# Kernel tuning notes

Hardware: AMD Instinct MI355X
Metric: run time of the kernel (lower is better)

Reference implementation:

```python
import jax, jax.numpy as jnp
import numpy as np
import math

# config constants (match init_kwargs)
H = 1024; NH = 16; NKV = 4; HD = 64; E = 16; I = 512
NG = 4; TKG = 2; TK = 4; ROUTED_SCALE = 2.5; EPS = 1e-6; THETA = 10000.0
B = 2; S = 1024


def setup_inputs() -> dict:
    key = jax.random.key(0)
    ks = jax.random.split(key, 16)
    sd = 0.02
    inp = {
        "hidden_states": jax.random.normal(ks[0], (B, S, H), jnp.float32),
        "position_ids": jnp.arange(B * S, dtype=jnp.int64).reshape(B, S) % 4096,
        "ln1_w": jnp.ones((H,), jnp.float32),
        "ln2_w": jnp.ones((H,), jnp.float32),
        "q_w": jax.random.normal(ks[1], (NH * HD, H), jnp.float32) * sd,
        "k_w": jax.random.normal(ks[2], (NKV * HD, H), jnp.float32) * sd,
        "v_w": jax.random.normal(ks[3], (NKV * HD, H), jnp.float32) * sd,
        "o_w": jax.random.normal(ks[4], (H, NH * HD), jnp.float32) * sd,
        "gate_w": jax.random.normal(ks[5], (E, H), jnp.float32) * sd,
        "e_bias": jax.random.normal(ks[6], (E,), jnp.float32) * 0.1,
        "W_gu": jax.random.normal(ks[7], (E, 2 * I, H), jnp.float32) * sd,
        "W_d": jax.random.normal(ks[8], (E, H, I), jnp.float32) * sd,
        "sg_w": jax.random.normal(ks[9], (2 * I, H), jnp.float32) * sd,
        "su_w": jax.random.normal(ks[10], (2 * I, H), jnp.float32) * sd,
        "sd_w": jax.random.normal(ks[11], (H, 2 * I), jnp.float32) * sd,
    }
    return inp


def _rmsnorm(x, w, eps=EPS):
    v = jnp.mean(x.astype(jnp.float32) ** 2, axis=-1, keepdims=True)
    return w * (x * jax.lax.rsqrt(v + eps)).astype(w.dtype)


def _rotate_half(x):
    x1, x2 = x[..., : HD // 2], x[..., HD // 2 :]
    return jnp.concatenate([-x2, x1], axis=-1)


def _attention(hs, position_ids, q_w, k_w, v_w, o_w):
    b, s, _ = hs.shape
    q = (hs @ q_w.T).reshape(b, s, NH, HD).transpose(0, 2, 1, 3)   # [B,NH,S,HD]
    k = (hs @ k_w.T).reshape(b, s, NKV, HD).transpose(0, 2, 1, 3)
    v = (hs @ v_w.T).reshape(b, s, NKV, HD).transpose(0, 2, 1, 3)
    # RoPE
    inv_freq = 1.0 / (THETA ** (jnp.arange(0, HD, 2, dtype=jnp.float32) / HD))
    freqs = position_ids.astype(jnp.float32)[..., None] * inv_freq  # [B,S,HD/2]
    emb = jnp.concatenate([freqs, freqs], axis=-1)                  # [B,S,HD]
    cos = jnp.cos(emb)[:, None]                                     # [B,1,S,HD]
    sin = jnp.sin(emb)[:, None]
    q = q * cos + _rotate_half(q) * sin
    k = k * cos + _rotate_half(k) * sin
    # GQA: repeat kv heads
    groups = NH // NKV
    k = jnp.repeat(k, groups, axis=1)
    v = jnp.repeat(v, groups, axis=1)
    scale = 1.0 / math.sqrt(HD)
    scores = jnp.einsum("bhsd,bhtd->bhst", q, k) * scale
    causal = jnp.triu(jnp.full((s, s), -jnp.inf, jnp.float32), k=1)
    scores = scores + causal[None, None]
    attn = jax.nn.softmax(scores.astype(jnp.float32), axis=-1).astype(q.dtype)
    out = jnp.einsum("bhst,bhtd->bhsd", attn, v)
    out = out.transpose(0, 2, 1, 3).reshape(b, s, NH * HD)
    return out @ o_w.T


def _moe(x, gate_w, e_bias, W_gu, W_d, sg_w, su_w, sd_w):
    b, s, h = x.shape
    xf = x.reshape(-1, h)                                     # [T,H]
    T = xf.shape[0]
    logits = xf.astype(jnp.float32) @ gate_w.astype(jnp.float32).T  # [T,E]
    scores = jax.nn.sigmoid(logits)
    sfc = scores + e_bias[None]
    # group-restricted top-k
    gsize = E // NG
    group_scores = sfc.reshape(T, NG, gsize).max(axis=-1)     # [T,NG]
    _, gidx = jax.lax.top_k(group_scores, TKG)                # [T,TKG]
    gmask = jnp.zeros((T, NG), bool).at[jnp.arange(T)[:, None], gidx].set(True)
    smask = jnp.repeat(gmask, gsize, axis=1)                  # [T,E]
    masked = jnp.where(smask, sfc, 0.0)
    _, topk_idx = jax.lax.top_k(masked, TK)                   # [T,TK]
    topk_w = jnp.take_along_axis(scores, topk_idx, axis=1)    # [T,TK]
    topk_w = topk_w / (topk_w.sum(axis=-1, keepdims=True) + 1e-20)
    topk_w = (topk_w * ROUTED_SCALE).astype(xf.dtype)
    # combine weights [T,E] (scatter-add over selected experts)
    combine = jnp.zeros((T, E), xf.dtype).at[
        jnp.arange(T)[:, None], topk_idx].add(topk_w)
    # dense expert compute (static shapes), weighted combine fused in einsum
    gu = jnp.einsum("th,eih->tei", xf, W_gu)                  # [T,E,2I]
    hidden = jax.nn.silu(gu[..., :I]) * gu[..., I:]           # [T,E,I]
    routed = jnp.einsum("tei,ehi,te->th", hidden, W_d, combine)
    # shared experts
    shared = ((jax.nn.silu(xf @ sg_w.T) * (xf @ su_w.T)) @ sd_w.T)
    return (routed + shared).reshape(b, s, h)


def reference(hidden_states, position_ids, ln1_w, ln2_w, q_w, k_w, v_w, o_w,
              gate_w, e_bias, W_gu, W_d, sg_w, su_w, sd_w):
    res = hidden_states
    hs = _rmsnorm(hidden_states, ln1_w)
    hs = res + _attention(hs, position_ids, q_w, k_w, v_w, o_w)
    res = hs
    hs = _rmsnorm(hs, ln2_w)
    hs = res + _moe(hs, gate_w, e_bias, W_gu, W_d, sg_w, su_w, sd_w)
    return hs
```

## Files before the change

### kernel.cpp

```cpp
#include <hip/hip_runtime.h>
#include <hip/hip_bf16.h>
#include <stdint.h>

typedef float f32x4 __attribute__((ext_vector_type(4)));
typedef short s16x8 __attribute__((ext_vector_type(8)));
typedef short s16x4 __attribute__((ext_vector_type(4)));

__device__ __forceinline__ short f2bf(float x) {
    union { float f; uint32_t u; } v; v.f = x;
    uint32_t r = v.u + 0x7fffu + ((v.u >> 16) & 1u);
    return (short)(r >> 16);
}
__device__ __forceinline__ float bf2f(short b) {
    union { uint32_t u; float f; } v; v.u = ((uint32_t)(uint16_t)b) << 16;
    return v.f;
}
__device__ __forceinline__ void gld16(const void* g, void* l) {
    __builtin_amdgcn_global_load_lds((const __attribute__((address_space(1))) uint32_t*)g,
                                     (__attribute__((address_space(3))) uint32_t*)l, 16, 0, 0);
}

__global__ __launch_bounds__(256) void cvt_all_kernel(const float* __restrict__ q, const float* __restrict__ k,
                                                      const float* __restrict__ v, const float* __restrict__ o,
                                                      const float* __restrict__ gu, const float* __restrict__ wd,
                                                      const float* __restrict__ sg, const float* __restrict__ su,
                                                      const float* __restrict__ sd, short* __restrict__ wqkv,
                                                      short* __restrict__ wo, short* __restrict__ wgu,
                                                      short* __restrict__ wdB, short* __restrict__ wsgsu,
                                                      short* __restrict__ wsd) {
    size_t i = (size_t)blockIdx.x * 256 + threadIdx.x;
    const float* src; short* dst;
    if (i < 655360) {
        if (i < 262144) { src = q + i * 4; dst = wqkv + i * 4; }
        else if (i < 327680) { src = k + (i - 262144) * 4; dst = wqkv + 1048576 + (i - 262144) * 4; }
        else if (i < 393216) { src = v + (i - 327680) * 4; dst = wqkv + 1310720 + (i - 327680) * 4; }
        else { src = o + (i - 393216) * 4; dst = wo + (i - 393216) * 4; }
    } else if (i < 6946816) {
        if (i < 4849664) { src = gu + (i - 655360) * 4; dst = wgu + (i - 655360) * 4; }
        else { src = wd + (i - 4849664) * 4; dst = wdB + (i - 4849664) * 4; }
    } else {
        if (i < 7208960) { src = sg + (i - 6946816) * 4; dst = wsgsu + (i - 6946816) * 4; }
        else if (i < 7471104) { src = su + (i - 7208960) * 4; dst = wsgsu + 1048576 + (i - 7208960) * 4; }
        else { src = sd + (i - 7471104) * 4; dst = wsd + (i - 7471104) * 4; }
    }
    f32x4 val = *(const f32x4*)src;
    s16x4 ov;
    ov[0] = f2bf(val[0]); ov[1] = f2bf(val[1]); ov[2] = f2bf(val[2]); ov[3] = f2bf(val[3]);
    *(s16x4*)dst = ov;
}

__global__ __launch_bounds__(256) void rmsnorm_kernel(const float* __restrict__ x, const float* __restrict__ w,
                                                      short* __restrict__ out) {
    int t = blockIdx.x;
    f32x4 v = ((const f32x4*)(x + (size_t)t * 1024))[threadIdx.x];
    float ssq = v[0]*v[0] + v[1]*v[1] + v[2]*v[2] + v[3]*v[3];
#pragma unroll
    for (int o = 1; o < 64; o <<= 1) ssq += __shfl_xor(ssq, o);
    __shared__ float red[4];
    if ((threadIdx.x & 63) == 0) red[threadIdx.x >> 6] = ssq;
    __syncthreads();
    float tot = red[0] + red[1] + red[2] + red[3];
    float rs = rsqrtf(tot * (1.0f / 1024.0f) + 1e-6f);
    f32x4 wv = ((const f32x4*)w)[threadIdx.x];
    s16x4 o4;
#pragma unroll
    for (int j = 0; j < 4; ++j) o4[j] = f2bf(v[j] * rs * wv[j]);
    ((s16x4*)(out + (size_t)t * 1024))[threadIdx.x] = o4;
}

__global__ __launch_bounds__(256) void addnorm_kernel(const float* __restrict__ a, const float* __restrict__ b,
                                                      const float* __restrict__ w, float* __restrict__ res,
                                                      short* __restrict__ xf, float* __restrict__ xf32) {
    int t = blockIdx.x;
    f32x4 va = ((const f32x4*)(a + (size_t)t * 1024))[threadIdx.x];
    f32x4 vb = ((const f32x4*)(b + (size_t)t * 1024))[threadIdx.x]
             + ((const f32x4*)(b + (size_t)2048 * 1024 + (size_t)t * 1024))[threadIdx.x];
    f32x4 s = va + vb;
    ((f32x4*)(res + (size_t)t * 1024))[threadIdx.x] = s;
    float ssq = s[0]*s[0] + s[1]*s[1] + s[2]*s[2] + s[3]*s[3];
#pragma unroll
    for (int o = 1; o < 64; o <<= 1) ssq += __shfl_xor(ssq, o);
    __shared__ float red[4];
    if ((threadIdx.x & 63) == 0) red[threadIdx.x >> 6] = ssq;
    __syncthreads();
    float tot = red[0] + red[1] + red[2] + red[3];
    float rs = rsqrtf(tot * (1.0f / 1024.0f) + 1e-6f);
    f32x4 wv = ((const f32x4*)w)[threadIdx.x];
    f32x4 xo;
    s16x4 o4;
#pragma unroll
    for (int j = 0; j < 4; ++j) { xo[j] = s[j] * rs * wv[j]; o4[j] = f2bf(xo[j]); }
    ((f32x4*)(xf32 + (size_t)t * 1024))[threadIdx.x] = xo;
    ((s16x4*)(xf + (size_t)t * 1024))[threadIdx.x] = o4;
}

__global__ __launch_bounds__(256, 4) void gemm2_kernel(const short* __restrict__ A, const short* __restrict__ Bg,
                                                       void* __restrict__ Cv, int M, int N, int Ktot, int Ksub,
                                                       const int* __restrict__ counts, const int* __restrict__ lists,
                                                       const int* __restrict__ plan, int a_shift, int store_bf16) {
    __shared__ short As[2][128 * 32];
    __shared__ short Bs[2][128 * 32];
    int e, bm, bn, k0, Mloc;
    size_t coff;
    const int* rl = nullptr;
    if (plan) {
        int wi = blockIdx.y;
        if (wi >= plan[0]) return;
        int it = plan[1 + wi];
        e = it & 31; bm = (it >> 5) * 128;
        bn = blockIdx.x * 128; k0 = 0;
        Mloc = counts[e]; rl = lists + e * 2048; coff = 0;
    } else {
        e = 0; bm = blockIdx.x * 128; bn = blockIdx.y * 128;
        k0 = blockIdx.z * Ksub; Mloc = M;
        coff = (size_t)blockIdx.z * M * N;
    }
    if (bm >= Mloc) return;
    const short* Bt = Bg + (size_t)e * N * Ktot;
    int tid = threadIdx.x, w = tid >> 6, l = tid & 63;
    int lr = l & 15, lg = l >> 4;
    int rsub = l >> 2, u = l & 3;
    int fs = (rsub & 3) ^ ((rsub >> 2) & 3);
    int colsel = (u ^ fs) * 8;
    int ra = w * 32 + rsub;
    int ga0 = bm + ra;       if (ga0 > Mloc - 1) ga0 = Mloc - 1;
    int ga1 = bm + ra + 16;  if (ga1 > Mloc - 1) ga1 = Mloc - 1;
    int ar0 = rl ? (rl[ga0] >> a_shift) : ga0;
    int ar1 = rl ? (rl[ga1] >> a_shift) : ga1;
    const short* Ap0 = A + (size_t)ar0 * Ktot + k0 + colsel;
    const short* Ap1 = A + (size_t)ar1 * Ktot + k0 + colsel;
    const short* Bp0 = Bt + (size_t)(bn + ra) * Ktot + k0 + colsel;
    const short* Bp1 = Bt + (size_t)(bn + ra + 16) * Ktot + k0 + colsel;
    int lb0 = w * 1024, lb1 = w * 1024 + 512;

    int wm = (w >> 1) * 64, wn = (w & 1) * 64;
    int su = lg ^ (lr & 3) ^ ((lr >> 2) & 3);
    int aoff[4], boff[4];
#pragma unroll
    for (int mf = 0; mf < 4; ++mf) aoff[mf] = (wm + mf * 16 + lr) * 32 + su * 8;
#pragma unroll
    for (int nf = 0; nf < 4; ++nf) boff[nf] = (wn + nf * 16 + lr) * 32 + su * 8;

    f32x4 zero4 = {0.f, 0.f, 0.f, 0.f};
    f32x4 acc[4][4];
#pragma unroll
    for (int mf = 0; mf < 4; ++mf)
#pragma unroll
        for (int nf = 0; nf < 4; ++nf) acc[mf][nf] = zero4;

#define STAGE(buf, kt) do { \
        gld16(Ap0 + (kt) * 32, &As[buf][lb0]); \
        gld16(Ap1 + (kt) * 32, &As[buf][lb1]); \
        gld16(Bp0 + (kt) * 32, &Bs[buf][lb0]); \
        gld16(Bp1 + (kt) * 32, &Bs[buf][lb1]); \
    } while (0)

    int nk = Ksub >> 5;
    STAGE(0, 0);
    asm volatile("s_waitcnt vmcnt(0)");
    __syncthreads();
    for (int kt = 0; kt < nk; ++kt) {
        int cur = kt & 1;
        if (kt + 1 < nk) STAGE(cur ^ 1, kt + 1);
        s16x8 af[4], bfr[4];
#pragma unroll
        for (int mf = 0; mf < 4; ++mf) af[mf] = *(const s16x8*)&As[cur][aoff[mf]];
#pragma unroll
        for (int nf = 0; nf < 4; ++nf) bfr[nf] = *(const s16x8*)&Bs[cur][boff[nf]];
#pragma unroll
        for (int mf = 0; mf < 4; ++mf)
#pragma unroll
            for (int nf = 0; nf < 4; ++nf)
                acc[mf][nf] = __builtin_amdgcn_mfma_f32_16x16x32_bf16(af[mf], bfr[nf], acc[mf][nf], 0, 0, 0);
        __syncthreads();
    }
#undef STAGE
    float* Cf = (float*)Cv;
    short* Cs = (short*)Cv;
#pragma unroll
    for (int mf = 0; mf < 4; ++mf) {
        int rbase = bm + wm + mf * 16 + lg * 4;
#pragma unroll
        for (int r = 0; r < 4; ++r) {
            int grow = rbase + r;
            if (grow < Mloc) {
                int crow = rl ? rl[grow] : grow;
                size_t cb = coff + (size_t)crow * N + bn + wn + lr;
                if (store_bf16) {
#pragma unroll
                    for (int nf = 0; nf < 4; ++nf) Cs[cb + nf * 16] = f2bf(acc[mf][nf][r]);
                } else {
#pragma unroll
                    for (int nf = 0; nf < 4; ++nf) Cf[cb + nf * 16] = acc[mf][nf][r];
                }
            }
        }
    }
}

__global__ __launch_bounds__(64) void rope_kernel(const float* __restrict__ qkv, short* __restrict__ Qr,
                                                  short* __restrict__ Kr, short* __restrict__ Vt) {
    int t = blockIdx.x;
    int b = t >> 10, s = t & 1023;
    int l = threadIdx.x;
    __shared__ float cs[32], sn[32], qrow[1024], krow[256], vrow[256];
    const f32x4* r0 = (const f32x4*)(qkv + (size_t)t * 1536);
    const f32x4* r1 = (const f32x4*)(qkv + (size_t)2048 * 1536 + (size_t)t * 1536);
#pragma unroll
    for (int i = 0; i < 4; ++i) ((f32x4*)qrow)[l + i * 64] = r0[l + i * 64] + r1[l + i * 64];
    ((f32x4*)krow)[l] = r0[256 + l] + r1[256 + l];
    ((f32x4*)vrow)[l] = r0[320 + l] + r1[320 + l];
    if (l < 32) {
        float fr = (float)t * exp2f(-(float)l * 0.41524101186f);
        cs[l] = cosf(fr); sn[l] = sinf(fr);
    }
    __syncthreads();
    int d = l;
    float c = cs[d & 31], sv = sn[d & 31];
#pragma unroll
    for (int h = 0; h < 16; ++h) {
        float x = qrow[h * 64 + d];
        float rot = (d < 32) ? -qrow[h * 64 + d + 32] : qrow[h * 64 + d - 32];
        Qr[((size_t)(b * 16 + h) * 1024 + s) * 64 + d] = f2bf((x * c + rot * sv) * 0.125f);
    }
#pragma unroll
    for (int h = 0; h < 4; ++h) {
        float x = krow[h * 64 + d];
        float rot = (d < 32) ? -krow[h * 64 + d + 32] : krow[h * 64 + d - 32];
        Kr[((size_t)(b * 4 + h) * 1024 + s) * 64 + d] = f2bf(x * c + rot * sv);
        Vt[((size_t)(b * 4 + h) * 64 + d) * 1024 + s] = f2bf(vrow[h * 64 + d]);
    }
}

__global__ __launch_bounds__(64) void attn_kernel(const short* __restrict__ Qr, const short* __restrict__ Kr,
                                                  const short* __restrict__ Vt, short* __restrict__ attn_out) {
    int qb = blockIdx.x;
    int hb = blockIdx.y;
    int b = hb >> 4, h = hb & 15, kv = h >> 2;
    int l = threadIdx.x;
    int lr = l & 15, lg = l >> 4;
    int q0 = qb * 16;
    __shared__ short Pl[16 * 32];
    const short* Qbase = Qr + ((size_t)(b * 16 + h) * 1024 + q0 + lr) * 64;
    s16x8 qf0 = *(const s16x8*)(Qbase + lg * 8);
    s16x8 qf1 = *(const s16x8*)(Qbase + 32 + lg * 8);
    const short* Kbase = Kr + (size_t)(b * 4 + kv) * 1024 * 64;
    const short* Vbase = Vt + (size_t)(b * 4 + kv) * 64 * 1024;

    f32x4 zero4 = {0.f, 0.f, 0.f, 0.f};
    f32x4 o[4];
#pragma unroll
    for (int dt = 0; dt < 4; ++dt) o[dt] = zero4;
    float m = -1e30f, lsum = 0.f;
    int nt = (q0 + 16 + 31) >> 5;
    for (int kt = 0; kt < nt; ++kt) {
        int k0 = kt * 32;
        f32x4 sc0 = zero4, sc1 = zero4;
        const short* Kr0 = Kbase + (size_t)(k0 + lr) * 64;
        s16x8 ka = *(const s16x8*)(Kr0 + lg * 8);
        sc0 = __builtin_amdgcn_mfma_f32_16x16x32_bf16(ka, qf0, sc0, 0, 0, 0);
        ka = *(const s16x8*)(Kr0 + 32 + lg * 8);
        sc0 = __builtin_amdgcn_mfma_f32_16x16x32_bf16(ka, qf1, sc0, 0, 0, 0);
        const short* Kr1 = Kbase + (size_t)(k0 + 16 + lr) * 64;
        ka = *(const s16x8*)(Kr1 + lg * 8);
        sc1 = __builtin_amdgcn_mfma_f32_16x16x32_bf16(ka, qf0, sc1, 0, 0, 0);
        ka = *(const s16x8*)(Kr1 + 32 + lg * 8);
        sc1 = __builtin_amdgcn_mfma_f32_16x16x32_bf16(ka, qf1, sc1, 0, 0, 0);
        if (kt == nt - 1) {
            int q = q0 + lr;
#pragma unroll
            for (int r = 0; r < 4; ++r) {
                if (k0 + lg * 4 + r > q) sc0[r] = -1e30f;
                if (k0 + 16 + lg * 4 + r > q) sc1[r] = -1e30f;
            }
        }
        float tm = fmaxf(fmaxf(fmaxf(sc0[0], sc0[1]), fmaxf(sc0[2], sc0[3])),
                         fmaxf(fmaxf(sc1[0], sc1[1]), fmaxf(sc1[2], sc1[3])));
        tm = fmaxf(tm, __shfl_xor(tm, 16));
        tm = fmaxf(tm, __shfl_xor(tm, 32));
        float newm = fmaxf(m, tm);
        float fac = __expf(m - newm);
        float p[8];
#pragma unroll
        for (int r = 0; r < 4; ++r) { p[r] = __expf(sc0[r] - newm); p[4 + r] = __expf(sc1[r] - newm); }
        float ts = ((p[0] + p[1]) + (p[2] + p[3])) + ((p[4] + p[5]) + (p[6] + p[7]));
        ts += __shfl_xor(ts, 16);
        ts += __shfl_xor(ts, 32);
        lsum = lsum * fac + ts;
        m = newm;
        s16x4 w0, w1;
#pragma unroll
        for (int r = 0; r < 4; ++r) { w0[r] = f2bf(p[r]); w1[r] = f2bf(p[4 + r]); }
        *(s16x4*)&Pl[lr * 32 + lg * 4] = w0;
        *(s16x4*)&Pl[lr * 32 + 16 + lg * 4] = w1;
#pragma unroll
        for (int dt = 0; dt < 4; ++dt) {
            const short* Vrow = Vbase + (size_t)(dt * 16 + lr) * 1024 + k0;
            s16x8 va = *(const s16x8*)(Vrow + lg * 8);
            s16x8 pf = *(const s16x8*)&Pl[lr * 32 + lg * 8];
            o[dt] *= fac;
            o[dt] = __builtin_amdgcn_mfma_f32_16x16x32_bf16(va, pf, o[dt], 0, 0, 0);
        }
    }
    float inv = 1.f / lsum;
    short* obase = attn_out + ((size_t)(b * 1024 + q0 + lr)) * 1024 + h * 64;
#pragma unroll
    for (int dt = 0; dt < 4; ++dt)
#pragma unroll
        for (int r = 0; r < 4; ++r) obase[dt * 16 + lg * 4 + r] = f2bf(o[dt][r] * inv);
}

__global__ __launch_bounds__(256) void router_topk_kernel(const float* __restrict__ x32, const float* __restrict__ gw,
                                                          const float* __restrict__ eb, float* __restrict__ tw,
                                                          int* __restrict__ tidx) {
    int t = blockIdx.x * 4 + (threadIdx.x >> 6);
    int l = threadIdx.x & 63;
    const float* x = x32 + (size_t)t * 1024;
    f32x4 xv[4];
#pragma unroll
    for (int j = 0; j < 4; ++j) xv[j] = *(const f32x4*)(x + j * 256 + l * 4);
    float acc[16];
#pragma unroll
    for (int e = 0; e < 16; ++e) {
        float a = 0.f;
#pragma unroll
        for (int j = 0; j < 4; ++j) {
            f32x4 g = *(const f32x4*)(gw + (size_t)e * 1024 + j * 256 + l * 4);
            a += xv[j][0]*g[0] + xv[j][1]*g[1] + xv[j][2]*g[2] + xv[j][3]*g[3];
        }
        acc[e] = a;
    }
#pragma unroll
    for (int e = 0; e < 16; ++e) {
#pragma unroll
        for (int o = 1; o < 64; o <<= 1) acc[e] += __shfl_xor(acc[e], o);
    }
    if (l == 0) {
        float score[16], sfc[16];
#pragma unroll
        for (int e = 0; e < 16; ++e) {
            score[e] = 1.f / (1.f + __expf(-acc[e]));
            sfc[e] = score[e] + eb[e];
        }
        float gs[4];
#pragma unroll
        for (int g = 0; g < 4; ++g)
            gs[g] = fmaxf(fmaxf(sfc[4 * g], sfc[4 * g + 1]), fmaxf(sfc[4 * g + 2], sfc[4 * g + 3]));
        int g1 = 0;
        for (int g = 1; g < 4; ++g) if (gs[g] > gs[g1]) g1 = g;
        int g2 = -1;
        for (int g = 0; g < 4; ++g) {
            if (g == g1) continue;
            if (g2 < 0 || gs[g] > gs[g2]) g2 = g;
        }
        float masked[16];
#pragma unroll
        for (int e = 0; e < 16; ++e) {
            int g = e >> 2;
            masked[e] = (g == g1 || g == g2) ? sfc[e] : 0.0f;
        }
        float tot = 1e-20f;
        int idx[4]; float wv[4];
        for (int k = 0; k < 4; ++k) {
            int bi = 0;
            float bv = -1e30f;
            for (int e2 = 0; e2 < 16; ++e2)
                if (masked[e2] > bv) { bv = masked[e2]; bi = e2; }
            idx[k] = bi;
            wv[k] = score[bi];
            masked[bi] = -1e30f;
            tot += wv[k];
        }
        for (int k = 0; k < 4; ++k) {
            tw[t * 4 + k] = wv[k] / tot * 2.5f;
            tidx[t * 4 + k] = idx[k];
        }
    }
}

__global__ __launch_bounds__(64) void router_lists_kernel(const int* __restrict__ tidx, int* __restrict__ counts,
                                                          int* __restrict__ lists) {
    int e = blockIdx.x;
    int l = threadIdx.x;
    int base = 0;
    for (int it = 0; it < 128; ++it) {
        int p = it * 64 + l;
        bool match = (tidx[p] == e);
        unsigned long long mask = __ballot(match);
        int pos = __popcll(mask & ((1ull << l) - 1ull));
        if (match) lists[e * 2048 + base + pos] = p;
        base += __popcll(mask);
    }
    if (l == 0) counts[e] = base;
}

__global__ void plan_kernel(const int* __restrict__ counts, int* __restrict__ plan) {
    if (threadIdx.x == 0) {
        int n = 0;
        for (int e = 0; e < 16; ++e) {
            int nb = (counts[e] + 127) >> 7;
            for (int m2 = 0; m2 < nb; ++m2) plan[1 + n++] = e | (m2 << 5);
        }
        plan[0] = n;
    }
}

__global__ __launch_bounds__(128) void silu_routed_kernel(const short* __restrict__ gu, short* __restrict__ hid) {
    int pr = blockIdx.x;
    int j = threadIdx.x * 4;
    s16x4 gv = *(const s16x4*)(gu + (size_t)pr * 1024 + j);
    s16x4 uv = *(const s16x4*)(gu + (size_t)pr * 1024 + 512 + j);
    s16x4 o;
#pragma unroll
    for (int k = 0; k < 4; ++k) {
        float gf = bf2f(gv[k]);
        o[k] = f2bf(gf / (1.f + __expf(-gf)) * bf2f(uv[k]));
    }
    *(s16x4*)(hid + (size_t)pr * 512 + j) = o;
}

__global__ __launch_bounds__(256) void silu_shared_kernel(const short* __restrict__ gu, short* __restrict__ h) {
    int t = blockIdx.x;
    int j = threadIdx.x * 4;
    s16x4 gv = *(const s16x4*)(gu + (size_t)t * 2048 + j);
    s16x4 uv = *(const s16x4*)(gu + (size_t)t * 2048 + 1024 + j);
    s16x4 o;
#pragma unroll
    for (int k = 0; k < 4; ++k) {
        float gf = bf2f(gv[k]);
        o[k] = f2bf(gf / (1.f + __expf(-gf)) * bf2f(uv[k]));
    }
    *(s16x4*)(h + (size_t)t * 1024 + j) = o;
}

__global__ __launch_bounds__(256) void combine_kernel(const float* __restrict__ res2, const float* __restrict__ sdp,
                                                      const short* __restrict__ slots, const float* __restrict__ tw,
                                                      float* __restrict__ out) {
    int t = blockIdx.x;
    int i = threadIdx.x;
    f32x4 a = ((const f32x4*)(res2 + (size_t)t * 1024))[i];
    f32x4 s0 = ((const f32x4*)(sdp + (size_t)t * 1024))[i];
    f32x4 s1 = ((const f32x4*)(sdp + (size_t)2048 * 1024 + (size_t)t * 1024))[i];
    f32x4 acc = a + s0 + s1;
#pragma unroll
    for (int s = 0; s < 4; ++s) {
        float w = tw[t * 4 + s];
        s16x4 d = ((const s16x4*)(slots + (size_t)(t * 4 + s) * 1024))[i];
#pragma unroll
        for (int j = 0; j < 4; ++j) acc[j] += bf2f(d[j]) * w;
    }
    ((f32x4*)(out + (size_t)t * 1024))[i] = acc;
}

extern "C" void kernel_launch(void* const* d_in, const int* in_sizes, int n_in,
                              void* d_out, int out_size, void* d_ws, size_t ws_size,
                              hipStream_t stream) {
    const float* hidden = (const float*)d_in[0];
    const float* ln1 = (const float*)d_in[2];
    const float* ln2 = (const float*)d_in[3];
    const float* qw = (const float*)d_in[4];
    const float* kw = (const float*)d_in[5];
    const float* vw = (const float*)d_in[6];
    const float* ow = (const float*)d_in[7];
    const float* gatew = (const float*)d_in[8];
    const float* ebias = (const float*)d_in[9];
    const float* wgu = (const float*)d_in[10];
    const float* wd = (const float*)d_in[11];
    const float* sgw = (const float*)d_in[12];
    const float* suw = (const float*)d_in[13];
    const float* sdw = (const float*)d_in[14];
    float* out = (float*)d_out;

    char* base = (char*)d_ws;
    size_t off = 0;
    auto alloc = [&](size_t bytes) -> char* {
        char* r = base + off;
        off += (bytes + 255) & ~(size_t)255;
        return r;
    };
    const size_t MB = 1u << 20;

    short* wqkv_b = (short*)alloc((size_t)1536 * 1024 * 2);
    short* wo_b   = (short*)alloc((size_t)1024 * 1024 * 2);
    short* wgu_b  = (short*)alloc((size_t)16 * 1024 * 1024 * 2);
    short* wd_b   = (short*)alloc((size_t)16 * 1024 * 512 * 2);
    short* wsgsu_b= (short*)alloc((size_t)2048 * 1024 * 2);
    short* wsd_b  = (short*)alloc((size_t)1024 * 1024 * 2);
    float* res2 = (float*)alloc((size_t)2048 * 1024 * 4);
    short* xf   = (short*)alloc((size_t)2048 * 1024 * 2);
    float* topkw = (float*)alloc(2048 * 4 * 4);
    int* tidx   = (int*)alloc(8192 * 4);
    int* counts = (int*)alloc(64);
    int* lists  = (int*)alloc(16 * 2048 * 4);
    int* plan   = (int*)alloc(512);
    short* gu_or_sgsu = (short*)alloc((size_t)8192 * 1024 * 2);
    short* shhid = (short*)alloc((size_t)2048 * 1024 * 2);
    short* hid   = (short*)alloc((size_t)8192 * 512 * 2);

    char* ov = alloc(50 * MB);
    short* xn1       = (short*)(ov);
    float* qkv_part  = (float*)(ov + 4 * MB);
    short* Qr        = (short*)(ov);
    short* Kr        = (short*)(ov + 28 * MB);
    short* Vt        = (short*)(ov + 29 * MB);
    short* attn_out  = (short*)(ov + 30 * MB);
    float* attnproj_part = (float*)(ov + 34 * MB);
    float* xf32      = (float*)(ov);
    short* down_slot = (short*)(ov + 8 * MB);
    float* sd_part   = (float*)(ov + 24 * MB);

    cvt_all_kernel<<<30208, 256, 0, stream>>>(qw, kw, vw, ow, wgu, wd, sgw, suw, sdw,
                                              wqkv_b, wo_b, wgu_b, wd_b, wsgsu_b, wsd_b);

    rmsnorm_kernel<<<2048, 256, 0, stream>>>(hidden, ln1, xn1);
    gemm2_kernel<<<dim3(16, 12, 2), 256, 0, stream>>>(xn1, wqkv_b, qkv_part, 2048, 1536, 1024, 512,
                                                      nullptr, nullptr, nullptr, 0, 0);
    rope_kernel<<<2048, 64, 0, stream>>>(qkv_part, Qr, Kr, Vt);
    attn_kernel<<<dim3(64, 32, 1), 64, 0, stream>>>(Qr, Kr, Vt, attn_out);
    gemm2_kernel<<<dim3(16, 8, 2), 256, 0, stream>>>(attn_out, wo_b, attnproj_part, 2048, 1024, 1024, 512,
                                                     nullptr, nullptr, nullptr, 0, 0);
    addnorm_kernel<<<2048, 256, 0, stream>>>(hidden, attnproj_part, ln2, res2, xf, xf32);

    router_topk_kernel<<<512, 256, 0, stream>>>(xf32, gatew, ebias, topkw, tidx);
    router_lists_kernel<<<16, 64, 0, stream>>>(tidx, counts, lists);
    plan_kernel<<<1, 64, 0, stream>>>(counts, plan);

    gemm2_kernel<<<dim3(16, 16, 1), 256, 0, stream>>>(xf, wsgsu_b, gu_or_sgsu, 2048, 2048, 1024, 1024,
                                                      nullptr, nullptr, nullptr, 0, 1);
    silu_shared_kernel<<<2048, 256, 0, stream>>>(gu_or_sgsu, shhid);

    gemm2_kernel<<<dim3(8, 80, 1), 256, 0, stream>>>(xf, wgu_b, gu_or_sgsu, 0, 1024, 1024, 1024,
                                                     counts, lists, plan, 2, 1);
    silu_routed_kernel<<<8192, 128, 0, stream>>>(gu_or_sgsu, hid);

    gemm2_kernel<<<dim3(8, 80, 1), 256, 0, stream>>>(hid, wd_b, down_slot, 0, 1024, 512, 512,
                                                     counts, lists, plan, 0, 1);
    gemm2_kernel<<<dim3(16, 8, 2), 256, 0, stream>>>(shhid, wsd_b, sd_part, 2048, 1024, 1024, 512,
                                                     nullptr, nullptr, nullptr, 0, 0);

    combine_kernel<<<2048, 256, 0, stream>>>(res2, sd_part, down_slot, topkw, out);

    (void)in_sizes; (void)n_in; (void)out_size; (void)ws_size;
}
```

Baseline: 325.4 us.

## Pair mirrored causal query tiles per attention block with double-buffered K/V loads

Each attention block now handles two 16-row query tiles, p and 63-p, so causal work is balanced across blocks and every K/V tile loaded is reused by both query tiles. K/V fragments for the next key tile are prefetched into registers (double buffer) while the current tile is computed, and the P scratch in LDS is padded to 40 shorts per row. The grid is halved, so there are fewer and longer blocks, and register pressure rises from the two accumulator sets plus the buffered K/V fragments.

```diff
diff --git a/kernel.cpp b/kernel.cpp
--- a/kernel.cpp
+++ b/kernel.cpp
@@ -232,82 +232,110 @@
     }
 }
 
+struct KV { s16x8 k[4]; s16x8 v[4]; };
+__device__ __forceinline__ void kv_load(KV& r, const short* Kb, const short* Vb, int k0, int lr, int lg) {
+    const short* K0 = Kb + (size_t)(k0 + lr) * 64 + lg * 8;
+    const short* K1 = Kb + (size_t)(k0 + 16 + lr) * 64 + lg * 8;
+    r.k[0] = *(const s16x8*)K0;
+    r.k[1] = *(const s16x8*)(K0 + 32);
+    r.k[2] = *(const s16x8*)K1;
+    r.k[3] = *(const s16x8*)(K1 + 32);
+#pragma unroll
+    for (int dt = 0; dt < 4; ++dt)
+        r.v[dt] = *(const s16x8*)(Vb + (size_t)(dt * 16 + lr) * 1024 + k0 + lg * 8);
+}
+__device__ __forceinline__ void chain_step(const KV& kv, s16x8 qf0, s16x8 qf1, f32x4* o,
+                                           float& m, float& lsum, short* Pl,
+                                           int lr, int lg, int k0, int qmask) {
+    f32x4 z = {0.f, 0.f, 0.f, 0.f};
+    f32x4 sc0 = z, sc1 = z;
+    sc0 = __builtin_amdgcn_mfma_f32_16x16x32_bf16(kv.k[0], qf0, sc0, 0, 0, 0);
+    sc0 = __builtin_amdgcn_mfma_f32_16x16x32_bf16(kv.k[1], qf1, sc0, 0, 0, 0);
+    sc1 = __builtin_amdgcn_mfma_f32_16x16x32_bf16(kv.k[2], qf0, sc1, 0, 0, 0);
+    sc1 = __builtin_amdgcn_mfma_f32_16x16x32_bf16(kv.k[3], qf1, sc1, 0, 0, 0);
+#pragma unroll
+    for (int r = 0; r < 4; ++r) {
+        if (k0 + lg * 4 + r > qmask) sc0[r] = -1e30f;
+        if (k0 + 16 + lg * 4 + r > qmask) sc1[r] = -1e30f;
+    }
+    float tm = fmaxf(fmaxf(fmaxf(sc0[0], sc0[1]), fmaxf(sc0[2], sc0[3])),
+                     fmaxf(fmaxf(sc1[0], sc1[1]), fmaxf(sc1[2], sc1[3])));
+    tm = fmaxf(tm, __shfl_xor(tm, 16));
+    tm = fmaxf(tm, __shfl_xor(tm, 32));
+    float newm = fmaxf(m, tm);
+    float fac = __expf(m - newm);
+    float p[8];
+#pragma unroll
+    for (int r = 0; r < 4; ++r) { p[r] = __expf(sc0[r] - newm); p[4 + r] = __expf(sc1[r] - newm); }
+    float ts = ((p[0] + p[1]) + (p[2] + p[3])) + ((p[4] + p[5]) + (p[6] + p[7]));
+    ts += __shfl_xor(ts, 16);
+    ts += __shfl_xor(ts, 32);
+    lsum = lsum * fac + ts;
+    m = newm;
+    s16x4 w0, w1;
+#pragma unroll
+    for (int r = 0; r < 4; ++r) { w0[r] = f2bf(p[r]); w1[r] = f2bf(p[4 + r]); }
+    *(s16x4*)&Pl[lr * 40 + lg * 4] = w0;
+    *(s16x4*)&Pl[lr * 40 + 16 + lg * 4] = w1;
+    s16x8 pf = *(const s16x8*)&Pl[lr * 40 + lg * 8];
+#pragma unroll
+    for (int dt = 0; dt < 4; ++dt) {
+        o[dt] *= fac;
+        o[dt] = __builtin_amdgcn_mfma_f32_16x16x32_bf16(kv.v[dt], pf, o[dt], 0, 0, 0);
+    }
+}
+
 __global__ __launch_bounds__(64) void attn_kernel(const short* __restrict__ Qr, const short* __restrict__ Kr,
                                                   const short* __restrict__ Vt, short* __restrict__ attn_out) {
-    int qb = blockIdx.x;
+    int p = blockIdx.x;
     int hb = blockIdx.y;
     int b = hb >> 4, h = hb & 15, kv = h >> 2;
     int l = threadIdx.x;
     int lr = l & 15, lg = l >> 4;
-    int q0 = qb * 16;
-    __shared__ short Pl[16 * 32];
-    const short* Qbase = Qr + ((size_t)(b * 16 + h) * 1024 + q0 + lr) * 64;
-    s16x8 qf0 = *(const s16x8*)(Qbase + lg * 8);
-    s16x8 qf1 = *(const s16x8*)(Qbase + 32 + lg * 8);
+    int q0A = p * 16, q0B = (63 - p) * 16;
+    __shared__ short PlA[16 * 40], PlB[16 * 40];
+    const short* Qh = Qr + (size_t)(b * 16 + h) * 1024 * 64;
+    s16x8 qA0 = *(const s16x8*)(Qh + (size_t)(q0A + lr) * 64 + lg * 8);
+    s16x8 qA1 = *(const s16x8*)(Qh + (size_t)(q0A + lr) * 64 + 32 + lg * 8);
+    s16x8 qB0 = *(const s16x8*)(Qh + (size_t)(q0B + lr) * 64 + lg * 8);
+    s16x8 qB1 = *(const s16x8*)(Qh + (size_t)(q0B + lr) * 64 + 32 + lg * 8);
     const short* Kbase = Kr + (size_t)(b * 4 + kv) * 1024 * 64;
     const short* Vbase = Vt + (size_t)(b * 4 + kv) * 64 * 1024;
 
     f32x4 zero4 = {0.f, 0.f, 0.f, 0.f};
-    f32x4 o[4];
-#pragma unroll
-    for (int dt = 0; dt < 4; ++dt) o[dt] = zero4;
-    float m = -1e30f, lsum = 0.f;
-    int nt = (q0 + 16 + 31) >> 5;
-    for (int kt = 0; kt < nt; ++kt) {
-        int k0 = kt * 32;
-        f32x4 sc0 = zero4, sc1 = zero4;
-        const short* Kr0 = Kbase + (size_t)(k0 + lr) * 64;
-        s16x8 ka = *(const s16x8*)(Kr0 + lg * 8);
-        sc0 = __builtin_amdgcn_mfma_f32_16x16x32_bf16(ka, qf0, sc0, 0, 0, 0);
-        ka = *(const s16x8*)(Kr0 + 32 + lg * 8);
-        sc0 = __builtin_amdgcn_mfma_f32_16x16x32_bf16(ka, qf1, sc0, 0, 0, 0);
-        const short* Kr1 = Kbase + (size_t)(k0 + 16 + lr) * 64;
-        ka = *(const s16x8*)(Kr1 + lg * 8);
-        sc1 = __builtin_amdgcn_mfma_f32_16x16x32_bf16(ka, qf0, sc1, 0, 0, 0);
-        ka = *(const s16x8*)(Kr1 + 32 + lg * 8);
-        sc1 = __builtin_amdgcn_mfma_f32_16x16x32_bf16(ka, qf1, sc1, 0, 0, 0);
-        if (kt == nt - 1) {
-            int q = q0 + lr;
-#pragma unroll
-            for (int r = 0; r < 4; ++r) {
-                if (k0 + lg * 4 + r > q) sc0[r] = -1e30f;
-                if (k0 + 16 + lg * 4 + r > q) sc1[r] = -1e30f;
-            }
-        }
-        float tm = fmaxf(fmaxf(fmaxf(sc0[0], sc0[1]), fmaxf(sc0[2], sc0[3])),
-                         fmaxf(fmaxf(sc1[0], sc1[1]), fmaxf(sc1[2], sc1[3])));
-        tm = fmaxf(tm, __shfl_xor(tm, 16));
-        tm = fmaxf(tm, __shfl_xor(tm, 32));
-        float newm = fmaxf(m, tm);
-        float fac = __expf(m - newm);
-        float p[8];
-#pragma unroll
-        for (int r = 0; r < 4; ++r) { p[r] = __expf(sc0[r] - newm); p[4 + r] = __expf(sc1[r] - newm); }
-        float ts = ((p[0] + p[1]) + (p[2] + p[3])) + ((p[4] + p[5]) + (p[6] + p[7]));
-        ts += __shfl_xor(ts, 16);
-        ts += __shfl_xor(ts, 32);
-        lsum = lsum * fac + ts;
-        m = newm;
-        s16x4 w0, w1;
-#pragma unroll
-        for (int r = 0; r < 4; ++r) { w0[r] = f2bf(p[r]); w1[r] = f2bf(p[4 + r]); }
-        *(s16x4*)&Pl[lr * 32 + lg * 4] = w0;
-        *(s16x4*)&Pl[lr * 32 + 16 + lg * 4] = w1;
-#pragma unroll
-        for (int dt = 0; dt < 4; ++dt) {
-            const short* Vrow = Vbase + (size_t)(dt * 16 + lr) * 1024 + k0;
-            s16x8 va = *(const s16x8*)(Vrow + lg * 8);
-            s16x8 pf = *(const s16x8*)&Pl[lr * 32 + lg * 8];
-            o[dt] *= fac;
-            o[dt] = __builtin_amdgcn_mfma_f32_16x16x32_bf16(va, pf, o[dt], 0, 0, 0);
-        }
-    }
-    float inv = 1.f / lsum;
-    short* obase = attn_out + ((size_t)(b * 1024 + q0 + lr)) * 1024 + h * 64;
+    f32x4 oA[4], oB[4];
+#pragma unroll
+    for (int dt = 0; dt < 4; ++dt) { oA[dt] = zero4; oB[dt] = zero4; }
+    float mA = -1e30f, lsA = 0.f, mB = -1e30f, lsB = 0.f;
+    int ntA = (q0A + 47) >> 5, ntB = (q0B + 47) >> 5;
+    int qmA = q0A + lr, qmB = q0B + lr;
+    const int BIG = 1 << 29;
+
+    KV b0, b1;
+    kv_load(b0, Kbase, Vbase, 0, lr, lg);
+    for (int kt = 0; kt < ntB; kt += 2) {
+        if (kt + 1 < ntB) kv_load(b1, Kbase, Vbase, (kt + 1) * 32, lr, lg);
+        if (kt < ntA) chain_step(b0, qA0, qA1, oA, mA, lsA, PlA, lr, lg, kt * 32,
+                                 (kt == ntA - 1) ? qmA : BIG);
+        chain_step(b0, qB0, qB1, oB, mB, lsB, PlB, lr, lg, kt * 32,
+                   (kt == ntB - 1) ? qmB : BIG);
+        if (kt + 1 >= ntB) break;
+        if (kt + 2 < ntB) kv_load(b0, Kbase, Vbase, (kt + 2) * 32, lr, lg);
+        if (kt + 1 < ntA) chain_step(b1, qA0, qA1, oA, mA, lsA, PlA, lr, lg, (kt + 1) * 32,
+                                     (kt + 1 == ntA - 1) ? qmA : BIG);
+        chain_step(b1, qB0, qB1, oB, mB, lsB, PlB, lr, lg, (kt + 1) * 32,
+                   (kt + 1 == ntB - 1) ? qmB : BIG);
+    }
+    float invA = 1.f / lsA, invB = 1.f / lsB;
+    short* oa = attn_out + ((size_t)(b * 1024 + q0A + lr)) * 1024 + h * 64;
+    short* ob = attn_out + ((size_t)(b * 1024 + q0B + lr)) * 1024 + h * 64;
 #pragma unroll
     for (int dt = 0; dt < 4; ++dt)
 #pragma unroll
-        for (int r = 0; r < 4; ++r) obase[dt * 16 + lg * 4 + r] = f2bf(o[dt][r] * inv);
+        for (int r = 0; r < 4; ++r) {
+            oa[dt * 16 + lg * 4 + r] = f2bf(oA[dt][r] * invA);
+            ob[dt * 16 + lg * 4 + r] = f2bf(oB[dt][r] * invB);
+        }
 }
 
 __global__ __launch_bounds__(256) void router_topk_kernel(const float* __restrict__ x32, const float* __restrict__ gw,
@@ -516,7 +544,7 @@
     gemm2_kernel<<<dim3(16, 12, 2), 256, 0, stream>>>(xn1, wqkv_b, qkv_part, 2048, 1536, 1024, 512,
                                                       nullptr, nullptr, nullptr, 0, 0);
     rope_kernel<<<2048, 64, 0, stream>>>(qkv_part, Qr, Kr, Vt);
-    attn_kernel<<<dim3(64, 32, 1), 64, 0, stream>>>(Qr, Kr, Vt, attn_out);
+    attn_kernel<<<dim3(32, 32, 1), 64, 0, stream>>>(Qr, Kr, Vt, attn_out);
     gemm2_kernel<<<dim3(16, 8, 2), 256, 0, stream>>>(attn_out, wo_b, attnproj_part, 2048, 1024, 1024, 512,
                                                      nullptr, nullptr, nullptr, 0, 0);
     addnorm_kernel<<<2048, 256, 0, stream>>>(hidden, attnproj_part, ln2, res2, xf, xf32);
```

Result: faster. 300.5 us (-7.6%).
